# Kernel tuning notes

Measured on AMD Instinct MI355X. Metric: run time of the kernel, lower is better.

## Reference

```python
import jax, jax.numpy as jnp
import numpy as np

S, B, C, OUT, H = 2048, 4, 1024, 1024, 16
D = OUT // H
SCALE = float(np.sqrt(D))


def setup_inputs() -> dict:
    key = jax.random.key(0)
    ks = jax.random.split(key, 5)
    return {
        "x": jax.random.normal(ks[0], (S, B, C), dtype=jnp.float32),
        "Wqkv": jax.random.normal(ks[1], (3 * OUT, C), dtype=jnp.float32) * 0.02,
        "bqkv": jax.random.normal(ks[2], (3 * OUT,), dtype=jnp.float32) * 0.02,
        "Wo": jax.random.normal(ks[3], (OUT, OUT), dtype=jnp.float32) * 0.02,
        "bo": jax.random.normal(ks[4], (OUT,), dtype=jnp.float32) * 0.02,
    }


def reference(x, Wqkv, bqkv, Wo, bo):
    s, b, _ = x.shape
    # qkv projection: (S, B, 3*OUT)
    qkv = x @ Wqkv.T + bqkv
    # (S, B, 3, H, D) -> (3, B, H, S, D)  [matches torch permute(2,1,3,0,4)]
    qkv = qkv.reshape(s, b, 3, H, D).transpose(2, 1, 3, 0, 4)
    q, k, v = qkv[0], qkv[1], qkv[2]
    # scores: (B, H, S, S)
    attn = jnp.einsum("bhsd,bhtd->bhst", q, k) / SCALE
    attn = jax.nn.softmax(attn, axis=-1)
    av = jnp.einsum("bhst,bhtd->bhsd", attn, v)  # (B, H, S, D)
    # faithful to torch: transpose(1,2) -> (B, S, H, D) then reshape(S, B, -1)
    y = jnp.swapaxes(av, 1, 2).reshape(s, b, H * D)
    return y @ Wo.T + bo
```

## Files before the change

kernel.cpp:

```cpp
#include <hip/hip_runtime.h>
#include <hip/hip_bf16.h>
#include <math.h>

#define S_LEN 2048
#define B_SZ 4
#define NH 16
#define HD 64
#define C_DIM 1024
#define OUT_DIM 1024

static constexpr size_t BHSD = (size_t)B_SZ * NH * S_LEN * HD;
#define QSCALE 0.18033688011112042f

typedef __attribute__((ext_vector_type(8))) short v8bf;
typedef __attribute__((ext_vector_type(4))) float v4f;
typedef __attribute__((ext_vector_type(4))) unsigned short v4us;

__device__ inline unsigned short f2bf(float x) {
    unsigned u = __float_as_uint(x);
    return (unsigned short)((u + 0x7fffu + ((u >> 16) & 1u)) >> 16);
}
__device__ inline float bf2f(unsigned short h) {
    return __uint_as_float(((unsigned)h) << 16);
}
__device__ inline unsigned short cvt_bf(float x) {
    __hip_bfloat16 hb = __float2bfloat16(x);
    return reinterpret_cast<unsigned short&>(hb);
}

__global__ __launch_bounds__(256)
void cvt_hl_kernel(const float* __restrict__ src, unsigned short* __restrict__ hi,
                   unsigned short* __restrict__ lo, int n4)
{
    int i = blockIdx.x * 256 + threadIdx.x;
    if (i >= n4) return;
    float4 v = reinterpret_cast<const float4*>(src)[i];
    float x[4] = {v.x, v.y, v.z, v.w};
    v4us h, l;
#pragma unroll
    for (int j = 0; j < 4; ++j) {
        unsigned short hh = f2bf(x[j]);
        h[j] = hh;
        l[j] = f2bf(x[j] - bf2f(hh));
    }
    reinterpret_cast<v4us*>(hi)[i] = h;
    reinterpret_cast<v4us*>(lo)[i] = l;
}

__global__ __launch_bounds__(256)
void cvt_hi_kernel(const float* __restrict__ src, unsigned short* __restrict__ hi, int n4)
{
    int i = blockIdx.x * 256 + threadIdx.x;
    if (i >= n4) return;
    float4 v = reinterpret_cast<const float4*>(src)[i];
    float x[4] = {v.x, v.y, v.z, v.w};
    v4us h;
#pragma unroll
    for (int j = 0; j < 4; ++j) h[j] = f2bf(x[j]);
    reinterpret_cast<v4us*>(hi)[i] = h;
}

__device__ __forceinline__ void split2_mainloop_r3(
    const unsigned short* __restrict__ Ahi, const unsigned short* __restrict__ Alo,
    const unsigned short* __restrict__ Bhi,
    int an0, int bm0, unsigned short* SA, unsigned short* SB, v4f acc[4][4])
{
    constexpr int K = 1024;
    constexpr int NT = K / 32;
    const int t = threadIdx.x;
    const int lane = t & 63;
    const int w = t >> 6;
    const int wm = w >> 1;
    const int wn = w & 1;
    const int lr = lane & 15, lg = lane >> 4;

    auto CHUNK = [&](int kt, int bf, int u) {
        const int k0 = kt * 32;
        const int c = w * 4 + u;
        const unsigned short* src;
        unsigned short* dst;
        if (c < 16) {
            int rt = c >> 1, par = c & 1;
            src = (par ? Alo : Ahi) + (size_t)(an0 + rt * 16 + lr) * K + k0 + lg * 8;
            dst = SA + bf * 8192 + par * 4096 + rt * 512;
        } else {
            int rt = c - 16;
            src = Bhi + (size_t)(bm0 + rt * 16 + lr) * K + k0 + lg * 8;
            dst = SB + bf * 8192 + rt * 512;
        }
        __builtin_amdgcn_global_load_lds(
            (const __attribute__((address_space(1))) unsigned int*)src,
            (__attribute__((address_space(3))) unsigned int*)dst, 16, 0, 0);
    };
    auto STAGE_ALL = [&](int kt, int bf) {
#pragma unroll
        for (int u = 0; u < 4; ++u) CHUNK(kt, bf, u);
    };

    STAGE_ALL(0, 0);
    STAGE_ALL(1, 1);

    for (int kt = 0; kt < NT; ++kt) {
        const int bf = kt % 3;
        if (kt + 1 < NT) { asm volatile("s_waitcnt vmcnt(4)" ::: "memory"); }
        else             { asm volatile("s_waitcnt vmcnt(0)" ::: "memory"); }
        __builtin_amdgcn_s_barrier();
        __builtin_amdgcn_sched_barrier(0);

        const unsigned short* sa = SA + bf * 8192;
        const unsigned short* sb = SB + bf * 8192;
        const bool pf = (kt + 2 < NT);
        const int bf2 = (kt + 2) % 3;

        v8bf ah[4], al[4], bh[4];

#pragma unroll
        for (int i = 0; i < 4; ++i) {
            ah[i] = *reinterpret_cast<const v8bf*>(sa + (wn * 4 + i) * 512 + lane * 8);
            al[i] = *reinterpret_cast<const v8bf*>(sa + 4096 + (wn * 4 + i) * 512 + lane * 8);
        }
#pragma unroll
        for (int q = 0; q < 2; ++q)
            bh[q] = *reinterpret_cast<const v8bf*>(sb + (wm * 4 + q) * 512 + lane * 8);
        if (pf) { CHUNK(kt + 2, bf2, 0); CHUNK(kt + 2, bf2, 1); }
        __builtin_amdgcn_s_barrier();
        asm volatile("s_waitcnt lgkmcnt(0)" ::: "memory");
        __builtin_amdgcn_sched_barrier(0);
        __builtin_amdgcn_s_setprio(1);
#pragma unroll
        for (int q = 0; q < 2; ++q) {
#pragma unroll
            for (int nt = 0; nt < 4; ++nt)
                acc[q][nt] = __builtin_amdgcn_mfma_f32_16x16x32_bf16(ah[nt], bh[q], acc[q][nt], 0, 0, 0);
#pragma unroll
            for (int nt = 0; nt < 4; ++nt)
                acc[q][nt] = __builtin_amdgcn_mfma_f32_16x16x32_bf16(al[nt], bh[q], acc[q][nt], 0, 0, 0);
        }
        __builtin_amdgcn_s_setprio(0);
        __builtin_amdgcn_s_barrier();
        __builtin_amdgcn_sched_barrier(0);

#pragma unroll
        for (int q = 2; q < 4; ++q)
            bh[q] = *reinterpret_cast<const v8bf*>(sb + (wm * 4 + q) * 512 + lane * 8);
        if (pf) { CHUNK(kt + 2, bf2, 2); CHUNK(kt + 2, bf2, 3); }
        __builtin_amdgcn_s_barrier();
        asm volatile("s_waitcnt lgkmcnt(0)" ::: "memory");
        __builtin_amdgcn_sched_barrier(0);
        __builtin_amdgcn_s_setprio(1);
#pragma unroll
        for (int q = 2; q < 4; ++q) {
#pragma unroll
            for (int nt = 0; nt < 4; ++nt)
                acc[q][nt] = __builtin_amdgcn_mfma_f32_16x16x32_bf16(ah[nt], bh[q], acc[q][nt], 0, 0, 0);
#pragma unroll
            for (int nt = 0; nt < 4; ++nt)
                acc[q][nt] = __builtin_amdgcn_mfma_f32_16x16x32_bf16(al[nt], bh[q], acc[q][nt], 0, 0, 0);
        }
        __builtin_amdgcn_s_setprio(0);
    }
}

__global__ __launch_bounds__(512, 2)
void qkv_gemm_mfma(const unsigned short* __restrict__ Whi, const unsigned short* __restrict__ Wlo,
                   const unsigned short* __restrict__ Xhi, const float* __restrict__ bias,
                   unsigned short* __restrict__ qb, unsigned short* __restrict__ kb,
                   unsigned short* __restrict__ vb)
{
    __shared__ __align__(16) unsigned short SA[3 * 8192];
    __shared__ __align__(16) unsigned short SB[3 * 8192];
    const v4f zero4 = {0.f, 0.f, 0.f, 0.f};
    v4f acc[4][4];
#pragma unroll
    for (int i = 0; i < 4; ++i)
#pragma unroll
        for (int j = 0; j < 4; ++j) acc[i][j] = zero4;

    const int bm0 = blockIdx.x * 256;
    const int an0 = blockIdx.y * 128;
    split2_mainloop_r3(Whi, Wlo, Xhi, an0, bm0, SA, SB, acc);

    const int t = threadIdx.x;
    const int lane = t & 63;
    const int w = t >> 6;
    const int wm = w >> 1, wn = w & 1;
    const int lr = lane & 15, lg = lane >> 4;
    const int nbase = an0 + wn * 64;
    const int mbase = bm0 + wm * 64;

#pragma unroll
    for (int nt = 0; nt < 4; ++nt) {
        const int n0 = nbase + nt * 16 + lg * 4;
        const float4 b4 = *reinterpret_cast<const float4*>(bias + n0);
        const float bv[4] = {b4.x, b4.y, b4.z, b4.w};
        const int tsel = n0 >> 10;
        const int np = n0 & 1023;
        const int hh = np >> 6;
        const int dd = np & 63;
#pragma unroll
        for (int mt = 0; mt < 4; ++mt) {
            const int m = mbase + mt * 16 + lr;
            const int s = m >> 2, b = m & 3;
            float vals[4];
#pragma unroll
            for (int r = 0; r < 4; ++r) vals[r] = acc[mt][nt][r] + bv[r];
            if (tsel == 0) {
                v4us h;
#pragma unroll
                for (int r = 0; r < 4; ++r) h[r] = f2bf(vals[r] * QSCALE);
                *reinterpret_cast<v4us*>(qb + ((size_t)(b * NH + hh) * S_LEN + s) * HD + dd) = h;
            } else if (tsel == 1) {
                v4us h;
#pragma unroll
                for (int r = 0; r < 4; ++r) h[r] = f2bf(vals[r]);
                *reinterpret_cast<v4us*>(kb + ((size_t)(b * NH + hh) * S_LEN + s) * HD + dd) = h;
            } else {
#pragma unroll
                for (int r = 0; r < 4; ++r)
                    vb[((size_t)(b * NH + hh) * HD + dd + r) * S_LEN + s] = f2bf(vals[r]);
            }
        }
    }
}

__global__ __launch_bounds__(256, 3)
void attn_kernel(const unsigned short* __restrict__ qb, const unsigned short* __restrict__ kb,
                 const unsigned short* __restrict__ vb, unsigned short* __restrict__ avh)
{
    __shared__ __align__(16) unsigned short SM[2][8192];
    __shared__ __align__(16) unsigned short PL[4][32 * 64];

    const int t = threadIdx.x;
    const int lane = t & 63;
    const int w = t >> 6;
    const int lr = lane & 15;
    const int lg = lane >> 4;
    const int id = blockIdx.x;
    const int bh = id & 63;
    const int qt = id >> 6;
    const int b = bh >> 4, h = bh & 15;
    const size_t bh_sd = (size_t)bh * (S_LEN * HD);
    const int q0 = qt * 128 + w * 32;
    char* const plw = (char*)&PL[w][0];
    const unsigned swz = (unsigned)((lr & 7) << 4);

    v8bf qh[2][2];
#pragma unroll
    for (int mt = 0; mt < 2; ++mt)
#pragma unroll
        for (int ks = 0; ks < 2; ++ks)
            qh[mt][ks] = *reinterpret_cast<const v8bf*>(
                qb + bh_sd + (size_t)(q0 + mt * 16 + lr) * HD + ks * 32 + lg * 8);

    auto STAGE = [&](int kt, int bf) {
#pragma unroll
        for (int u = 0; u < 4; ++u) {
            int cid = w * 4 + u;
            const unsigned short* src;
            unsigned short* dst;
            if (cid < 8) {
                int nt = cid >> 1, kn = cid & 1;
                src = kb + bh_sd + (size_t)(kt * 64 + nt * 16 + lr) * HD + kn * 32 + lg * 8;
                dst = &SM[bf][cid * 512];
            } else {
                int n = cid - 8;
                int nt = n >> 1, kn = n & 1;
                src = vb + bh_sd + (size_t)(nt * 16 + lr) * S_LEN + kt * 64 + kn * 32 + lg * 8;
                dst = &SM[bf][4096 + n * 512];
            }
            __builtin_amdgcn_global_load_lds(
                (const __attribute__((address_space(1))) unsigned int*)src,
                (__attribute__((address_space(3))) unsigned int*)dst, 16, 0, 0);
        }
    };

    const v4f zero4 = {0.f, 0.f, 0.f, 0.f};
    v4f O[2][4];
    float m_run[2], l_run[2];
#pragma unroll
    for (int mt = 0; mt < 2; ++mt) { m_run[mt] = -1e30f; l_run[mt] = 0.f; }
#pragma unroll
    for (int mt = 0; mt < 2; ++mt)
#pragma unroll
        for (int nt = 0; nt < 4; ++nt) O[mt][nt] = zero4;

    constexpr int NT = S_LEN / 64;

    STAGE(0, 0);
    asm volatile("s_waitcnt vmcnt(0)" ::: "memory");
    __builtin_amdgcn_s_barrier();
    __builtin_amdgcn_sched_barrier(0);

    for (int kt = 0; kt < NT; ++kt) {
        const int cur = kt & 1;
        if (kt + 1 < NT) STAGE(kt + 1, cur ^ 1);

        const unsigned short* KB = &SM[cur][0];
        const unsigned short* VT = &SM[cur][4096];

        v4f sc[2][4];
#pragma unroll
        for (int mt = 0; mt < 2; ++mt)
#pragma unroll
            for (int nt = 0; nt < 4; ++nt) sc[mt][nt] = zero4;
        __builtin_amdgcn_s_setprio(1);
#pragma unroll
        for (int ks = 0; ks < 2; ++ks)
#pragma unroll
            for (int nt = 0; nt < 4; ++nt) {
                v8bf kh = *reinterpret_cast<const v8bf*>(KB + (nt * 2 + ks) * 512 + lane * 8);
#pragma unroll
                for (int mt = 0; mt < 2; ++mt)
                    sc[mt][nt] = __builtin_amdgcn_mfma_f32_16x16x32_bf16(kh, qh[mt][ks], sc[mt][nt], 0, 0, 0);
            }
        __builtin_amdgcn_s_setprio(0);

        float rm[2];
        bool need = false;
#pragma unroll
        for (int mt = 0; mt < 2; ++mt) {
            float lm = -1e30f;
#pragma unroll
            for (int nt = 0; nt < 4; ++nt)
#pragma unroll
                for (int r = 0; r < 4; ++r) lm = fmaxf(lm, sc[mt][nt][r]);
            lm = fmaxf(lm, __shfl_xor(lm, 16));
            lm = fmaxf(lm, __shfl_xor(lm, 32));
            rm[mt] = lm;
            need = need || (lm > m_run[mt] + 8.0f);
        }
        if (__any(need)) {
#pragma unroll
            for (int mt = 0; mt < 2; ++mt) {
                float nm = fmaxf(m_run[mt], rm[mt]);
                float alpha = __builtin_amdgcn_exp2f(m_run[mt] - nm);
                m_run[mt] = nm;
                l_run[mt] *= alpha;
                float af[4];
#pragma unroll
                for (int r = 0; r < 4; ++r) af[r] = __shfl(alpha, lg * 4 + r);
#pragma unroll
                for (int nt = 0; nt < 4; ++nt)
#pragma unroll
                    for (int r = 0; r < 4; ++r) O[mt][nt][r] *= af[r];
            }
        }
#pragma unroll
        for (int mt = 0; mt < 2; ++mt) {
            float rs = 0.f;
#pragma unroll
            for (int nt = 0; nt < 4; ++nt) {
                v4us pp;
#pragma unroll
                for (int r = 0; r < 4; ++r) {
                    float p = __builtin_amdgcn_exp2f(sc[mt][nt][r] - m_run[mt]);
                    rs += p;
                    pp[r] = cvt_bf(p);
                }
                unsigned wb = (unsigned)((mt * 16 + lr) * 128 + (nt * 16 + lg * 4) * 2) ^ swz;
                *reinterpret_cast<v4us*>(plw + wb) = pp;
            }
            rs += __shfl_xor(rs, 16);
            rs += __shfl_xor(rs, 32);
            l_run[mt] += rs;
        }
        asm volatile("s_waitcnt lgkmcnt(0)" ::: "memory");
        __builtin_amdgcn_sched_barrier(0);

        __builtin_amdgcn_s_setprio(1);
#pragma unroll
        for (int ks = 0; ks < 2; ++ks) {
            v8bf pa[2];
#pragma unroll
            for (int mt = 0; mt < 2; ++mt) {
                unsigned rb = (unsigned)((mt * 16 + lr) * 128 + (ks * 32 + lg * 8) * 2) ^ swz;
                pa[mt] = *reinterpret_cast<const v8bf*>(plw + rb);
            }
#pragma unroll
            for (int nt = 0; nt < 4; ++nt) {
                v8bf vf = *reinterpret_cast<const v8bf*>(VT + (nt * 2 + ks) * 512 + lane * 8);
#pragma unroll
                for (int mt = 0; mt < 2; ++mt)
                    O[mt][nt] = __builtin_amdgcn_mfma_f32_16x16x32_bf16(pa[mt], vf, O[mt][nt], 0, 0, 0);
            }
        }
        __builtin_amdgcn_s_setprio(0);

        asm volatile("s_waitcnt vmcnt(0)" ::: "memory");
        __builtin_amdgcn_s_barrier();
        __builtin_amdgcn_sched_barrier(0);
    }

#pragma unroll
    for (int mt = 0; mt < 2; ++mt) {
        float linv = 1.f / l_run[mt];
#pragma unroll
        for (int r = 0; r < 4; ++r) {
            float inv = __shfl(linv, lg * 4 + r);
            int s = q0 + mt * 16 + lg * 4 + r;
            size_t base = (size_t)(b * S_LEN + s) * OUT_DIM + h * HD;
#pragma unroll
            for (int nt = 0; nt < 4; ++nt)
                avh[base + nt * 16 + lr] = cvt_bf(O[mt][nt][r] * inv);
        }
    }
}

__global__ __launch_bounds__(512, 2)
void out_gemm_mfma(const unsigned short* __restrict__ Whi, const unsigned short* __restrict__ Wlo,
                   const unsigned short* __restrict__ Bhi, const float* __restrict__ bias,
                   float* __restrict__ out)
{
    __shared__ __align__(16) unsigned short SA[3 * 8192];
    __shared__ __align__(16) unsigned short SB[3 * 8192];
    const v4f zero4 = {0.f, 0.f, 0.f, 0.f};
    v4f acc[4][4];
#pragma unroll
    for (int i = 0; i < 4; ++i)
#pragma unroll
        for (int j = 0; j < 4; ++j) acc[i][j] = zero4;

    const int bm0 = blockIdx.x * 256;
    const int an0 = blockIdx.y * 128;
    split2_mainloop_r3(Whi, Wlo, Bhi, an0, bm0, SA, SB, acc);

    const int t = threadIdx.x;
    const int lane = t & 63;
    const int w = t >> 6;
    const int wm = w >> 1, wn = w & 1;
    const int lr = lane & 15, lg = lane >> 4;
    const int nbase = an0 + wn * 64;
    const int mbase = bm0 + wm * 64;

#pragma unroll
    for (int nt = 0; nt < 4; ++nt) {
        const int n0 = nbase + nt * 16 + lg * 4;
        const float4 b4 = *reinterpret_cast<const float4*>(bias + n0);
#pragma unroll
        for (int mt = 0; mt < 4; ++mt) {
            const int m = mbase + mt * 16 + lr;
            float4 o = make_float4(acc[mt][nt][0] + b4.x, acc[mt][nt][1] + b4.y,
                                   acc[mt][nt][2] + b4.z, acc[mt][nt][3] + b4.w);
            *reinterpret_cast<float4*>(out + (size_t)m * OUT_DIM + n0) = o;
        }
    }
}

extern "C" void kernel_launch(void* const* d_in, const int* in_sizes, int n_in,
                              void* d_out, int out_size, void* d_ws, size_t ws_size,
                              hipStream_t stream)
{
    const float* x    = (const float*)d_in[0];
    const float* Wqkv = (const float*)d_in[1];
    const float* bqkv = (const float*)d_in[2];
    const float* Wo   = (const float*)d_in[3];
    const float* bo   = (const float*)d_in[4];
    float* out = (float*)d_out;

    unsigned short* p = (unsigned short*)d_ws;
    unsigned short* xhi = p;            p += BHSD;
    unsigned short* wqh = p;            p += 3 * OUT_DIM * C_DIM;
    unsigned short* wql = p;            p += 3 * OUT_DIM * C_DIM;
    unsigned short* woh = p;            p += OUT_DIM * OUT_DIM;
    unsigned short* wol = p;            p += OUT_DIM * OUT_DIM;
    unsigned short* qb = p;             p += BHSD;
    unsigned short* kb = p;             p += BHSD;
    unsigned short* vb = p;             p += BHSD;
    unsigned short* avh = xhi;

    cvt_hi_kernel<<<dim3((int)(BHSD / 4 / 256)), 256, 0, stream>>>(x, xhi, (int)(BHSD / 4));
    cvt_hl_kernel<<<dim3(3 * OUT_DIM * C_DIM / 4 / 256), 256, 0, stream>>>(Wqkv, wqh, wql, 3 * OUT_DIM * C_DIM / 4);
    cvt_hl_kernel<<<dim3(OUT_DIM * C_DIM / 4 / 256), 256, 0, stream>>>(Wo, woh, wol, OUT_DIM * C_DIM / 4);

    qkv_gemm_mfma<<<dim3(32, 24), 512, 0, stream>>>(wqh, wql, xhi, bqkv, qb, kb, vb);
    attn_kernel<<<dim3(1024), 256, 0, stream>>>(qb, kb, vb, avh);
    out_gemm_mfma<<<dim3(32, 8), 512, 0, stream>>>(woh, wol, avh, bo, out);
}
```

Baseline: 273.7 us.

## Shrink GEMM tiles to 128x128 with 256-thread blocks and simplified pipeline

Both projection GEMMs now use 128x128 output tiles with 4 waves instead of 256x128 with 8 waves, doubling the grid. The mainloop issues all six async global-to-LDS chunks for stage kt+2 at the top of each iteration. It also loads all B fragments at once and drops the split half-step barriers. This is meant to improve load balance and wave count on the GPU and cut barrier overhead, at the cost of less data reuse per block and more global traffic.

```diff
diff --git a/kernel.cpp b/kernel.cpp
--- a/kernel.cpp
+++ b/kernel.cpp
@@ -60,7 +60,7 @@
     reinterpret_cast<v4us*>(hi)[i] = h;
 }
 
-__device__ __forceinline__ void split2_mainloop_r3(
+__device__ __forceinline__ void split2_mainloop_128(
     const unsigned short* __restrict__ Ahi, const unsigned short* __restrict__ Alo,
     const unsigned short* __restrict__ Bhi,
     int an0, int bm0, unsigned short* SA, unsigned short* SB, v4f acc[4][4])
@@ -76,7 +76,7 @@
 
     auto CHUNK = [&](int kt, int bf, int u) {
         const int k0 = kt * 32;
-        const int c = w * 4 + u;
+        const int c = w * 6 + u;
         const unsigned short* src;
         unsigned short* dst;
         if (c < 16) {
@@ -86,7 +86,7 @@
         } else {
             int rt = c - 16;
             src = Bhi + (size_t)(bm0 + rt * 16 + lr) * K + k0 + lg * 8;
-            dst = SB + bf * 8192 + rt * 512;
+            dst = SB + bf * 4096 + rt * 512;
         }
         __builtin_amdgcn_global_load_lds(
             (const __attribute__((address_space(1))) unsigned int*)src,
@@ -94,7 +94,7 @@
     };
     auto STAGE_ALL = [&](int kt, int bf) {
 #pragma unroll
-        for (int u = 0; u < 4; ++u) CHUNK(kt, bf, u);
+        for (int u = 0; u < 6; ++u) CHUNK(kt, bf, u);
     };
 
     STAGE_ALL(0, 0);
@@ -102,33 +102,25 @@
 
     for (int kt = 0; kt < NT; ++kt) {
         const int bf = kt % 3;
-        if (kt + 1 < NT) { asm volatile("s_waitcnt vmcnt(4)" ::: "memory"); }
+        if (kt + 1 < NT) { asm volatile("s_waitcnt vmcnt(6)" ::: "memory"); }
         else             { asm volatile("s_waitcnt vmcnt(0)" ::: "memory"); }
         __builtin_amdgcn_s_barrier();
         __builtin_amdgcn_sched_barrier(0);
 
+        if (kt + 2 < NT) STAGE_ALL(kt + 2, (kt + 2) % 3);
+
         const unsigned short* sa = SA + bf * 8192;
-        const unsigned short* sb = SB + bf * 8192;
-        const bool pf = (kt + 2 < NT);
-        const int bf2 = (kt + 2) % 3;
-
+        const unsigned short* sb = SB + bf * 4096;
         v8bf ah[4], al[4], bh[4];
-
 #pragma unroll
         for (int i = 0; i < 4; ++i) {
             ah[i] = *reinterpret_cast<const v8bf*>(sa + (wn * 4 + i) * 512 + lane * 8);
             al[i] = *reinterpret_cast<const v8bf*>(sa + 4096 + (wn * 4 + i) * 512 + lane * 8);
-        }
-#pragma unroll
-        for (int q = 0; q < 2; ++q)
-            bh[q] = *reinterpret_cast<const v8bf*>(sb + (wm * 4 + q) * 512 + lane * 8);
-        if (pf) { CHUNK(kt + 2, bf2, 0); CHUNK(kt + 2, bf2, 1); }
-        __builtin_amdgcn_s_barrier();
-        asm volatile("s_waitcnt lgkmcnt(0)" ::: "memory");
-        __builtin_amdgcn_sched_barrier(0);
+            bh[i] = *reinterpret_cast<const v8bf*>(sb + (wm * 4 + i) * 512 + lane * 8);
+        }
         __builtin_amdgcn_s_setprio(1);
 #pragma unroll
-        for (int q = 0; q < 2; ++q) {
+        for (int q = 0; q < 4; ++q) {
 #pragma unroll
             for (int nt = 0; nt < 4; ++nt)
                 acc[q][nt] = __builtin_amdgcn_mfma_f32_16x16x32_bf16(ah[nt], bh[q], acc[q][nt], 0, 0, 0);
@@ -137,38 +129,17 @@
                 acc[q][nt] = __builtin_amdgcn_mfma_f32_16x16x32_bf16(al[nt], bh[q], acc[q][nt], 0, 0, 0);
         }
         __builtin_amdgcn_s_setprio(0);
-        __builtin_amdgcn_s_barrier();
-        __builtin_amdgcn_sched_barrier(0);
-
-#pragma unroll
-        for (int q = 2; q < 4; ++q)
-            bh[q] = *reinterpret_cast<const v8bf*>(sb + (wm * 4 + q) * 512 + lane * 8);
-        if (pf) { CHUNK(kt + 2, bf2, 2); CHUNK(kt + 2, bf2, 3); }
-        __builtin_amdgcn_s_barrier();
-        asm volatile("s_waitcnt lgkmcnt(0)" ::: "memory");
-        __builtin_amdgcn_sched_barrier(0);
-        __builtin_amdgcn_s_setprio(1);
-#pragma unroll
-        for (int q = 2; q < 4; ++q) {
-#pragma unroll
-            for (int nt = 0; nt < 4; ++nt)
-                acc[q][nt] = __builtin_amdgcn_mfma_f32_16x16x32_bf16(ah[nt], bh[q], acc[q][nt], 0, 0, 0);
-#pragma unroll
-            for (int nt = 0; nt < 4; ++nt)
-                acc[q][nt] = __builtin_amdgcn_mfma_f32_16x16x32_bf16(al[nt], bh[q], acc[q][nt], 0, 0, 0);
-        }
-        __builtin_amdgcn_s_setprio(0);
-    }
-}
-
-__global__ __launch_bounds__(512, 2)
+    }
+}
+
+__global__ __launch_bounds__(256, 2)
 void qkv_gemm_mfma(const unsigned short* __restrict__ Whi, const unsigned short* __restrict__ Wlo,
                    const unsigned short* __restrict__ Xhi, const float* __restrict__ bias,
                    unsigned short* __restrict__ qb, unsigned short* __restrict__ kb,
                    unsigned short* __restrict__ vb)
 {
     __shared__ __align__(16) unsigned short SA[3 * 8192];
-    __shared__ __align__(16) unsigned short SB[3 * 8192];
+    __shared__ __align__(16) unsigned short SB[3 * 4096];
     const v4f zero4 = {0.f, 0.f, 0.f, 0.f};
     v4f acc[4][4];
 #pragma unroll
@@ -176,9 +147,9 @@
 #pragma unroll
         for (int j = 0; j < 4; ++j) acc[i][j] = zero4;
 
-    const int bm0 = blockIdx.x * 256;
+    const int bm0 = blockIdx.x * 128;
     const int an0 = blockIdx.y * 128;
-    split2_mainloop_r3(Whi, Wlo, Xhi, an0, bm0, SA, SB, acc);
+    split2_mainloop_128(Whi, Wlo, Xhi, an0, bm0, SA, SB, acc);
 
     const int t = threadIdx.x;
     const int lane = t & 63;
@@ -406,13 +377,13 @@
     }
 }
 
-__global__ __launch_bounds__(512, 2)
+__global__ __launch_bounds__(256, 2)
 void out_gemm_mfma(const unsigned short* __restrict__ Whi, const unsigned short* __restrict__ Wlo,
                    const unsigned short* __restrict__ Bhi, const float* __restrict__ bias,
                    float* __restrict__ out)
 {
     __shared__ __align__(16) unsigned short SA[3 * 8192];
-    __shared__ __align__(16) unsigned short SB[3 * 8192];
+    __shared__ __align__(16) unsigned short SB[3 * 4096];
     const v4f zero4 = {0.f, 0.f, 0.f, 0.f};
     v4f acc[4][4];
 #pragma unroll
@@ -420,9 +391,9 @@
 #pragma unroll
         for (int j = 0; j < 4; ++j) acc[i][j] = zero4;
 
-    const int bm0 = blockIdx.x * 256;
+    const int bm0 = blockIdx.x * 128;
     const int an0 = blockIdx.y * 128;
-    split2_mainloop_r3(Whi, Wlo, Bhi, an0, bm0, SA, SB, acc);
+    split2_mainloop_128(Whi, Wlo, Bhi, an0, bm0, SA, SB, acc);
 
     const int t = threadIdx.x;
     const int lane = t & 63;
@@ -472,7 +443,7 @@
     cvt_hl_kernel<<<dim3(3 * OUT_DIM * C_DIM / 4 / 256), 256, 0, stream>>>(Wqkv, wqh, wql, 3 * OUT_DIM * C_DIM / 4);
     cvt_hl_kernel<<<dim3(OUT_DIM * C_DIM / 4 / 256), 256, 0, stream>>>(Wo, woh, wol, OUT_DIM * C_DIM / 4);
 
-    qkv_gemm_mfma<<<dim3(32, 24), 512, 0, stream>>>(wqh, wql, xhi, bqkv, qb, kb, vb);
+    qkv_gemm_mfma<<<dim3(64, 24), 256, 0, stream>>>(wqh, wql, xhi, bqkv, qb, kb, vb);
     attn_kernel<<<dim3(1024), 256, 0, stream>>>(qb, kb, vb, avh);
-    out_gemm_mfma<<<dim3(32, 8), 512, 0, stream>>>(woh, wol, avh, bo, out);
-}
+    out_gemm_mfma<<<dim3(64, 8), 256, 0, stream>>>(woh, wol, avh, bo, out);
+}
```

After: 310.6 us. +13.5%, slower.
